# Kernel optimization log

Measured on AMD Instinct MI355X. Metric: run time of the kernel, lower is better.

## Reference

```python
import jax, jax.numpy as jnp
import numpy as np

SIGMA = 1.0
E_THETA = 0.1
E_ALPHA = 1.0
T = 750   # hardcoded by the original loop `for i in range(750)`
W = 11    # window width, loop `for j in range(11)`


def _pad(a):
    # Replicates the torch padding: [first*6, a, last*5] -> length T+11.
    # (The torch code writes last-6 slots then overwrites index T+5 with the
    #  middle slice; net effect is 6 copies of first, 5 copies of last.)
    return jnp.concatenate(
        [jnp.repeat(a[:, :1], 6, axis=1), a, jnp.repeat(a[:, -1:], 5, axis=1)],
        axis=1,
    )


def setup_inputs() -> dict:
    key = jax.random.key(0)
    k1, k2 = jax.random.split(key)
    B = 4096
    return {
        "actioness": jax.random.uniform(k1, (B, T), dtype=jnp.float32),
        "actioness_2": jax.random.uniform(k2, (B, T), dtype=jnp.float32),
    }


def reference(actioness, actioness_2):
    a0, a2 = actioness, actioness_2      # [B, T]
    p0, p2 = _pad(a0), _pad(a2)          # [B, T+11]
    win0 = jnp.stack([p0[:, j:j + T] for j in range(W)], axis=-1)  # [B, T, 11]
    win2 = jnp.stack([p2[:, j:j + T] for j in range(W)], axis=-1)  # [B, T, 11]
    # Gaussian-style weight from actioness similarity
    w = jnp.exp(-jnp.abs(a0[:, :, None] - win0) / (2.0 * SIGMA * SIGMA))
    loss = jnp.sum(w * jnp.abs(a2[:, :, None] - win2))
    # L2 regularizer: per-row L2 norm of the difference, summed over batch
    loss = loss + E_THETA * jnp.sum(jnp.linalg.norm(a0 - a2, axis=1))
    return loss * E_ALPHA
```

## Files before the change

kernel.cpp:

```cpp
#include <hip/hip_runtime.h>
#include <math.h>


#define T_LEN 750
#define BLK   256
#define CPT   3
#define NACT  (T_LEN / CPT)
#define SPAD  756
#define L2E_HALF 0.72134752044f

__global__ __launch_bounds__(BLK) void actloss_partial(
    const float* __restrict__ a0, const float* __restrict__ a2,
    float* __restrict__ partials)
{
    __shared__ float s0[SPAD];
    __shared__ float s2[SPAD];

    const int b   = blockIdx.x;
    const int tid = threadIdx.x;
    const float* __restrict__ g0 = a0 + (size_t)b * T_LEN;
    const float* __restrict__ g2 = a2 + (size_t)b * T_LEN;

    {
        const float2* __restrict__ v0 = (const float2*)g0;
        const float2* __restrict__ v2 = (const float2*)g2;
        for (int k = tid; k < 375; k += BLK) {
            const float2 x0 = v0[k];
            const float2 x2 = v2[k];
            s0[2 * k]     = x0.x;
            s0[2 * k + 1] = x0.y;
            s2[2 * k]     = x2.x;
            s2[2 * k + 1] = x2.y;
        }
        if (tid < SPAD - T_LEN) {
            s0[T_LEN + tid] = g0[T_LEN - 1];
            s2[T_LEN + tid] = g2[T_LEN - 1];
        }
    }
    __syncthreads();

    float loss1 = 0.0f;
    float loss2 = 0.0f;
    float sq    = 0.0f;

    if (tid < NACT) {
        const int i0 = tid * CPT;
        float r0[CPT + 6], r2[CPT + 6];
#pragma unroll
        for (int k = 0; k < CPT + 6; ++k) {
            r0[k] = s0[i0 + k];
            r2[k] = s2[i0 + k];
        }
#pragma unroll
        for (int ci = 0; ci < CPT; ++ci) {
            const float c0 = r0[ci];
            const float c2 = r2[ci];
#pragma unroll
            for (int k = 1; k <= 6; ++k) {
                const float wv  = __builtin_amdgcn_exp2f(
                                      -L2E_HALF * fabsf(c0 - r0[ci + k]));
                float ad2 = fabsf(c2 - r2[ci + k]);
                ad2 = (i0 + ci + k < T_LEN) ? ad2 : 0.0f;
                if (k <= 4) loss2 = fmaf(wv, ad2, loss2);
                else        loss1 = fmaf(wv, ad2, loss1);
            }
            const float d = c0 - c2;
            sq = fmaf(d, d, sq);
        }
    } else if (tid == NACT) {
#pragma unroll
        for (int i = 1; i <= 5; ++i) {
            const float wv = __builtin_amdgcn_exp2f(-L2E_HALF * fabsf(s0[i] - s0[0]));
            loss1 = fmaf(wv * (float)(6 - i), fabsf(s2[i] - s2[0]), loss1);
        }
#pragma unroll
        for (int i = 746; i <= 748; ++i) {
            const float wv = __builtin_amdgcn_exp2f(-L2E_HALF * fabsf(s0[i] - s0[T_LEN - 1]));
            loss1 = fmaf(wv * (float)(i - 745), fabsf(s2[i] - s2[T_LEN - 1]), loss1);
        }
    }

    float loss = fmaf(2.0f, loss2, loss1);

#pragma unroll
    for (int off = 32; off > 0; off >>= 1) {
        loss += __shfl_down(loss, off, 64);
        sq   += __shfl_down(sq,   off, 64);
    }
    __shared__ float rl[BLK / 64], rs[BLK / 64];
    const int wid  = tid >> 6;
    const int lane = tid & 63;
    if (lane == 0) { rl[wid] = loss; rs[wid] = sq; }
    __syncthreads();
    if (tid == 0) {
        float L = 0.0f, S = 0.0f;
#pragma unroll
        for (int w = 0; w < BLK / 64; ++w) { L += rl[w]; S += rs[w]; }
        partials[b] = L + 0.1f * sqrtf(S);
    }
}

__global__ __launch_bounds__(BLK) void actloss_final(
    const float* __restrict__ partials, int n4, float* __restrict__ out)
{
    const float4* __restrict__ p4 = (const float4*)partials;
    float v = 0.0f;
    for (int k = threadIdx.x; k < n4; k += BLK) {
        const float4 x = p4[k];
        v += (x.x + x.y) + (x.z + x.w);
    }
#pragma unroll
    for (int off = 32; off > 0; off >>= 1) v += __shfl_down(v, off, 64);
    __shared__ float r[BLK / 64];
    if ((threadIdx.x & 63) == 0) r[threadIdx.x >> 6] = v;
    __syncthreads();
    if (threadIdx.x == 0) {
        float s = 0.0f;
#pragma unroll
        for (int w = 0; w < BLK / 64; ++w) s += r[w];
        out[0] = s;
    }
}

extern "C" void kernel_launch(void* const* d_in, const int* in_sizes, int n_in,
                              void* d_out, int out_size, void* d_ws, size_t ws_size,
                              hipStream_t stream)
{
    const float* a0 = (const float*)d_in[0];
    const float* a2 = (const float*)d_in[1];
    float* out      = (float*)d_out;
    float* partials = (float*)d_ws;
    const int B = in_sizes[0] / T_LEN;

    actloss_partial<<<B, BLK, 0, stream>>>(a0, a2, partials);
    actloss_final<<<1, BLK, 0, stream>>>(partials, B / 4, out);
}
```

Baseline: 74.55 us.

## Process four rows per block to amortize block overhead and reductions

Each block now loads and processes four batch rows instead of one, which cuts the grid from B to B/4 blocks and runs one block-level reduction per four rows. Per-row squared sums are kept separately so the L2 norm per row stays correct. The goal is to amortize launch, sync and reduction overhead and to give each thread more independent work. In exchange, shared memory per block grows fourfold, and the grid drops to 1024 blocks, which may lower occupancy or leave CUs poorly balanced.

```diff
diff --git a/kernel.cpp b/kernel.cpp
--- a/kernel.cpp
+++ b/kernel.cpp
@@ -3,6 +3,7 @@
 
 
 #define T_LEN 750
+#define ROWS  4
 #define BLK   256
 #define CPT   3
 #define NACT  (T_LEN / CPT)
@@ -13,70 +14,78 @@
     const float* __restrict__ a0, const float* __restrict__ a2,
     float* __restrict__ partials)
 {
-    __shared__ float s0[SPAD];
-    __shared__ float s2[SPAD];
+    __shared__ float s0[ROWS][SPAD];
+    __shared__ float s2[ROWS][SPAD];
 
-    const int b   = blockIdx.x;
     const int tid = threadIdx.x;
-    const float* __restrict__ g0 = a0 + (size_t)b * T_LEN;
-    const float* __restrict__ g2 = a2 + (size_t)b * T_LEN;
+    const size_t base = (size_t)blockIdx.x * ROWS * T_LEN;
+    const float* __restrict__ g0 = a0 + base;
+    const float* __restrict__ g2 = a2 + base;
 
     {
         const float2* __restrict__ v0 = (const float2*)g0;
         const float2* __restrict__ v2 = (const float2*)g2;
-        for (int k = tid; k < 375; k += BLK) {
+        for (int k = tid; k < ROWS * 375; k += BLK) {
+            const int row  = k / 375;
+            const int col2 = 2 * (k - row * 375);
             const float2 x0 = v0[k];
             const float2 x2 = v2[k];
-            s0[2 * k]     = x0.x;
-            s0[2 * k + 1] = x0.y;
-            s2[2 * k]     = x2.x;
-            s2[2 * k + 1] = x2.y;
+            s0[row][col2]     = x0.x;
+            s0[row][col2 + 1] = x0.y;
+            s2[row][col2]     = x2.x;
+            s2[row][col2 + 1] = x2.y;
         }
-        if (tid < SPAD - T_LEN) {
-            s0[T_LEN + tid] = g0[T_LEN - 1];
-            s2[T_LEN + tid] = g2[T_LEN - 1];
+        if (tid < ROWS * (SPAD - T_LEN)) {
+            const int row = tid / (SPAD - T_LEN);
+            const int c   = tid - row * (SPAD - T_LEN);
+            s0[row][T_LEN + c] = g0[row * T_LEN + T_LEN - 1];
+            s2[row][T_LEN + c] = g2[row * T_LEN + T_LEN - 1];
         }
     }
     __syncthreads();
 
     float loss1 = 0.0f;
     float loss2 = 0.0f;
-    float sq    = 0.0f;
+    float sq[ROWS] = {0.0f, 0.0f, 0.0f, 0.0f};
 
     if (tid < NACT) {
         const int i0 = tid * CPT;
-        float r0[CPT + 6], r2[CPT + 6];
 #pragma unroll
-        for (int k = 0; k < CPT + 6; ++k) {
-            r0[k] = s0[i0 + k];
-            r2[k] = s2[i0 + k];
+        for (int r = 0; r < ROWS; ++r) {
+            float r0[CPT + 6], r2[CPT + 6];
+#pragma unroll
+            for (int k = 0; k < CPT + 6; ++k) {
+                r0[k] = s0[r][i0 + k];
+                r2[k] = s2[r][i0 + k];
+            }
+#pragma unroll
+            for (int ci = 0; ci < CPT; ++ci) {
+                const float c0 = r0[ci];
+                const float c2 = r2[ci];
+#pragma unroll
+                for (int k = 1; k <= 6; ++k) {
+                    const float wv  = __builtin_amdgcn_exp2f(
+                                          -L2E_HALF * fabsf(c0 - r0[ci + k]));
+                    float ad2 = fabsf(c2 - r2[ci + k]);
+                    ad2 = (i0 + ci + k < T_LEN) ? ad2 : 0.0f;
+                    if (k <= 4) loss2 = fmaf(wv, ad2, loss2);
+                    else        loss1 = fmaf(wv, ad2, loss1);
+                }
+                const float d = c0 - c2;
+                sq[r] = fmaf(d, d, sq[r]);
+            }
         }
-#pragma unroll
-        for (int ci = 0; ci < CPT; ++ci) {
-            const float c0 = r0[ci];
-            const float c2 = r2[ci];
-#pragma unroll
-            for (int k = 1; k <= 6; ++k) {
-                const float wv  = __builtin_amdgcn_exp2f(
-                                      -L2E_HALF * fabsf(c0 - r0[ci + k]));
-                float ad2 = fabsf(c2 - r2[ci + k]);
-                ad2 = (i0 + ci + k < T_LEN) ? ad2 : 0.0f;
-                if (k <= 4) loss2 = fmaf(wv, ad2, loss2);
-                else        loss1 = fmaf(wv, ad2, loss1);
-            }
-            const float d = c0 - c2;
-            sq = fmaf(d, d, sq);
-        }
-    } else if (tid == NACT) {
+    } else if (tid < NACT + ROWS) {
+        const int r = tid - NACT;
 #pragma unroll
         for (int i = 1; i <= 5; ++i) {
-            const float wv = __builtin_amdgcn_exp2f(-L2E_HALF * fabsf(s0[i] - s0[0]));
-            loss1 = fmaf(wv * (float)(6 - i), fabsf(s2[i] - s2[0]), loss1);
+            const float wv = __builtin_amdgcn_exp2f(-L2E_HALF * fabsf(s0[r][i] - s0[r][0]));
+            loss1 = fmaf(wv * (float)(6 - i), fabsf(s2[r][i] - s2[r][0]), loss1);
         }
 #pragma unroll
         for (int i = 746; i <= 748; ++i) {
-            const float wv = __builtin_amdgcn_exp2f(-L2E_HALF * fabsf(s0[i] - s0[T_LEN - 1]));
-            loss1 = fmaf(wv * (float)(i - 745), fabsf(s2[i] - s2[T_LEN - 1]), loss1);
+            const float wv = __builtin_amdgcn_exp2f(-L2E_HALF * fabsf(s0[r][i] - s0[r][T_LEN - 1]));
+            loss1 = fmaf(wv * (float)(i - 745), fabsf(s2[r][i] - s2[r][T_LEN - 1]), loss1);
         }
     }
 
@@ -85,18 +94,32 @@
 #pragma unroll
     for (int off = 32; off > 0; off >>= 1) {
         loss += __shfl_down(loss, off, 64);
-        sq   += __shfl_down(sq,   off, 64);
+#pragma unroll
+        for (int r = 0; r < ROWS; ++r) sq[r] += __shfl_down(sq[r], off, 64);
     }
-    __shared__ float rl[BLK / 64], rs[BLK / 64];
+    __shared__ float rl[BLK / 64];
+    __shared__ float rs[BLK / 64][ROWS];
     const int wid  = tid >> 6;
     const int lane = tid & 63;
-    if (lane == 0) { rl[wid] = loss; rs[wid] = sq; }
+    if (lane == 0) {
+        rl[wid] = loss;
+#pragma unroll
+        for (int r = 0; r < ROWS; ++r) rs[wid][r] = sq[r];
+    }
     __syncthreads();
     if (tid == 0) {
-        float L = 0.0f, S = 0.0f;
+        float L = 0.0f;
+        float S[ROWS] = {0.0f, 0.0f, 0.0f, 0.0f};
 #pragma unroll
-        for (int w = 0; w < BLK / 64; ++w) { L += rl[w]; S += rs[w]; }
-        partials[b] = L + 0.1f * sqrtf(S);
+        for (int w = 0; w < BLK / 64; ++w) {
+            L += rl[w];
+#pragma unroll
+            for (int r = 0; r < ROWS; ++r) S[r] += rs[w][r];
+        }
+        float reg = 0.0f;
+#pragma unroll
+        for (int r = 0; r < ROWS; ++r) reg += sqrtf(S[r]);
+        partials[blockIdx.x] = L + 0.1f * reg;
     }
 }
 
@@ -131,7 +154,8 @@
     float* out      = (float*)d_out;
     float* partials = (float*)d_ws;
     const int B = in_sizes[0] / T_LEN;
+    const int nblk = B / ROWS;
 
-    actloss_partial<<<B, BLK, 0, stream>>>(a0, a2, partials);
-    actloss_final<<<1, BLK, 0, stream>>>(partials, B / 4, out);
+    actloss_partial<<<nblk, BLK, 0, stream>>>(a0, a2, partials);
+    actloss_final<<<1, BLK, 0, stream>>>(partials, nblk / 4, out);
 }
```

Result: no change. 75.46 us (+1.2%).
